# Optimization experiments

Hardware: AMD Instinct MI355X
Metric: run time of the kernel (lower is better)

Reference implementation:

```python
import jax, jax.numpy as jnp
import numpy as np

N0, N1, N2 = 500000, 50000, 4096
E0, E1 = 1280000, 40960
IN, HID, OUT = 128, 256, 47


def _seg_mean(msg, dst, n):
    # scatter-mean of messages into n target buckets
    s = jax.ops.segment_sum(msg, dst, num_segments=n)
    cnt = jax.ops.segment_sum(jnp.ones((dst.shape[0],), msg.dtype), dst, num_segments=n)
    return s / jnp.maximum(cnt, 1.0)[:, None]


def _sage_conv(x_src, x_tgt, src, dst, W_l, b_l, W_r, n_tgt):
    # PyG SAGEConv (mean aggr): lin_l(mean_j x_j) + lin_r(x_i); bias on lin_l only
    agg = _seg_mean(x_src[src], dst, n_tgt)           # [n_tgt, d_in]
    return agg @ W_l + b_l + x_tgt @ W_r              # [n_tgt, d_out]


def setup_inputs() -> dict:
    key = jax.random.key(0)
    ks = jax.random.split(key, 9)
    inp = {
        "x": jax.random.normal(ks[0], (N0, IN), dtype=jnp.float32),
        "W_l0": jax.random.normal(ks[1], (IN, HID), dtype=jnp.float32) / np.sqrt(IN),
        "b_l0": jnp.zeros((HID,), dtype=jnp.float32),
        "W_r0": jax.random.normal(ks[2], (IN, HID), dtype=jnp.float32) / np.sqrt(IN),
        "W_l1": jax.random.normal(ks[3], (HID, OUT), dtype=jnp.float32) / np.sqrt(HID),
        "b_l1": jnp.zeros((OUT,), dtype=jnp.float32),
        "W_r1": jax.random.normal(ks[4], (HID, OUT), dtype=jnp.float32) / np.sqrt(HID),
        "src0": jax.random.randint(ks[5], (E0,), 0, N0, dtype=jnp.int32),
        "dst0": jax.random.randint(ks[6], (E0,), 0, N1, dtype=jnp.int32),
        "src1": jax.random.randint(ks[7], (E1,), 0, N1, dtype=jnp.int32),
        "dst1": jax.random.randint(ks[8], (E1,), 0, N2, dtype=jnp.int32),
        "n1": N1,
        "n2": N2,
    }
    return inp


def reference(x, W_l0, b_l0, W_r0, W_l1, b_l1, W_r1, src0, dst0, src1, dst1, n1, n2):
    # layer 0: bipartite conv (N0 sources -> n1 targets), relu (dropout: eval mode)
    h = _sage_conv(x, x[:n1], src0, dst0, W_l0, b_l0, W_r0, n1)
    h = jax.nn.relu(h)
    # layer 1: (n1 sources -> n2 targets)
    out = _sage_conv(h, h[:n2], src1, dst1, W_l1, b_l1, W_r1, n2)
    return jax.nn.log_softmax(out, axis=-1)
```

## Files before the change

### kernel.cpp

```cpp
#include <hip/hip_runtime.h>
#include <math.h>

typedef unsigned int u32;
typedef short bf16x8 __attribute__((ext_vector_type(8)));
typedef float f32x4 __attribute__((ext_vector_type(4)));

#define N0V 500000
#define N1V 50000
#define N2V 4096
#define E0V 1280000
#define E1V 40960
#define INF 128
#define HIDF 256
#define OUTF 47

#define HIST_BLOCKS 5160
#define PACKW_BLOCKS 128
#define USEDT_BLOCKS 16
#define USEDS_BLOCKS 160

#define NB0 196
#define NB1 16

__device__ __forceinline__ u32 bf16rne(float f) {
  u32 u = __float_as_uint(f);
  return (u + 0x7fffu + ((u >> 16) & 1u)) >> 16;
}
__device__ __forceinline__ u32 pk2(float lo, float hi) {
  return bf16rne(lo) | (bf16rne(hi) << 16);
}

__global__ __launch_bounds__(256) void prep_k(
    const int* __restrict__ dst0, const int* __restrict__ dst1,
    const int* __restrict__ src1,
    int* __restrict__ hist0, int* __restrict__ hist1, int* __restrict__ used,
    const float* __restrict__ Wl, const float* __restrict__ Wr,
    u32* __restrict__ Wf) {
  const int b = blockIdx.x;
  const int tid = threadIdx.x;
  if (b < HIST_BLOCKS) {
    int gid = b * 256 + tid;
    if (gid < E0V) {
      atomicAdd(&hist0[dst0[gid]], 1);
    } else {
      atomicAdd(&hist1[dst1[gid - E0V]], 1);
    }
  } else if (b < HIST_BLOCKS + PACKW_BLOCKS) {
    int gid = (b - HIST_BLOCKS) * 256 + tid;
    int e0 = 2 * gid;
    int j = e0 & 7;
    int lane = (e0 >> 3) & 63;
    int sq = e0 >> 9;
    int s = sq & 7;
    int t = sq >> 3;
    int n = t * 16 + (lane & 15);
    int k0 = s * 32 + (lane >> 4) * 8 + j;
    float v0 = (k0 < 128) ? Wl[k0 * 256 + n] : Wr[(k0 - 128) * 256 + n];
    float v1 = (k0 + 1 < 128) ? Wl[(k0 + 1) * 256 + n] : Wr[(k0 + 1 - 128) * 256 + n];
    Wf[gid] = pk2(v0, v1);
  } else if (b < HIST_BLOCKS + PACKW_BLOCKS + USEDT_BLOCKS) {
    int gid = (b - HIST_BLOCKS - PACKW_BLOCKS) * 256 + tid;
    used[gid] = 1;
  } else {
    int gid = (b - HIST_BLOCKS - PACKW_BLOCKS - USEDT_BLOCKS) * 256 + tid;
    used[src1[gid]] = 1;
  }
}

__global__ __launch_bounds__(256) void scanpart_k(
    const int* __restrict__ hist0, const int* __restrict__ hist1,
    const int* __restrict__ used,
    int* __restrict__ blkpc, int* __restrict__ blku, int* __restrict__ blk1) {
  __shared__ int sA[256], sB[256];
  const int b = blockIdx.x, t = threadIdx.x;
  if (b < NB0) {
    int i = b * 256 + t;
    int pc = 0, u = 0;
    if (i < N1V) {
      u = used[i];
      pc = u ? ((hist0[i] + 15) & ~15) : 0;
    }
    sA[t] = pc; sB[t] = u;
    __syncthreads();
    for (int off = 128; off > 0; off >>= 1) {
      if (t < off) { sA[t] += sA[t + off]; sB[t] += sB[t + off]; }
      __syncthreads();
    }
    if (t == 0) { blkpc[b] = sA[0]; blku[b] = sB[0]; }
  } else {
    int i = (b - NB0) * 256 + t;
    sA[t] = hist1[i];
    __syncthreads();
    for (int off = 128; off > 0; off >>= 1) {
      if (t < off) sA[t] += sA[t + off];
      __syncthreads();
    }
    if (t == 0) blk1[b - NB0] = sA[0];
  }
}

__global__ __launch_bounds__(256) void scanapply_k(
    const int* __restrict__ hist0, const int* __restrict__ hist1,
    const int* __restrict__ used,
    const int* __restrict__ blkpc, const int* __restrict__ blku,
    const int* __restrict__ blk1,
    int* __restrict__ poff, int* __restrict__ cntc,
    int* __restrict__ rowof, int* __restrict__ map,
    int* __restrict__ cur0, int* __restrict__ off1, int* __restrict__ cur1,
    int* __restrict__ Ucnt) {
  __shared__ int sA[256], sB[256];
  const int b = blockIdx.x, t = threadIdx.x;
  if (b < NB0) {
    sA[t] = (t < NB0) ? blkpc[t] : 0;
    sB[t] = (t < NB0) ? blku[t] : 0;
    __syncthreads();
    for (int off = 1; off < 256; off <<= 1) {
      int va = (t >= off) ? sA[t - off] : 0;
      int vb = (t >= off) ? sB[t - off] : 0;
      __syncthreads();
      sA[t] += va; sB[t] += vb;
      __syncthreads();
    }
    int base_pc = (b > 0) ? sA[b - 1] : 0;
    int base_u  = (b > 0) ? sB[b - 1] : 0;
    int total_pc = sA[255];
    int U = sB[255];
    __syncthreads();
    int i = b * 256 + t;
    int u = 0, n = 0, pc = 0;
    if (i < N1V) {
      u = used[i];
      n = u ? hist0[i] : 0;
      pc = u ? ((n + 15) & ~15) : 0;
    }
    sA[t] = pc; sB[t] = u;
    __syncthreads();
    for (int off = 1; off < 256; off <<= 1) {
      int va = (t >= off) ? sA[t - off] : 0;
      int vb = (t >= off) ? sB[t - off] : 0;
      __syncthreads();
      sA[t] += va; sB[t] += vb;
      __syncthreads();
    }
    if (u) {
      int j = base_u + sB[t] - u;
      int p = base_pc + sA[t] - pc;
      map[i] = j;
      rowof[j] = i;
      poff[j] = p;
      cntc[j] = n;
      cur0[i] = p;
    }
    if (b == NB0 - 1 && t == 0) {
      Ucnt[0] = U;
      for (int k = 0; k <= 16; k++) poff[U + k] = total_pc;
      for (int k = 0; k < 16; k++) cntc[U + k] = 0;
    }
  } else {
    int bb = b - NB0;
    sA[t] = (t < NB1) ? blk1[t] : 0;
    __syncthreads();
    for (int off = 1; off < 256; off <<= 1) {
      int va = (t >= off) ? sA[t - off] : 0;
      __syncthreads();
      sA[t] += va;
      __syncthreads();
    }
    int base = (bb > 0) ? sA[bb - 1] : 0;
    int total = sA[255];
    __syncthreads();
    int i = bb * 256 + t;
    int c = hist1[i];
    sA[t] = c;
    __syncthreads();
    for (int off = 1; off < 256; off <<= 1) {
      int va = (t >= off) ? sA[t - off] : 0;
      __syncthreads();
      sA[t] += va;
      __syncthreads();
    }
    int o = base + sA[t] - c;
    off1[i] = o; cur1[i] = o;
    if (bb == NB1 - 1 && t == 255) off1[N2V] = total;
  }
}

__global__ __launch_bounds__(256) void scatteridx_k(
    const int* __restrict__ src0, const int* __restrict__ dst0,
    const int* __restrict__ src1, const int* __restrict__ dst1,
    const int* __restrict__ used, const int* __restrict__ map,
    int* __restrict__ cur0, int* __restrict__ cur1,
    int* __restrict__ esrc0, int* __restrict__ esrc1) {
  int gid = blockIdx.x * 256 + threadIdx.x;
  if (gid < E0V) {
    int d = dst0[gid];
    if (used[d]) {
      int pos = atomicAdd(&cur0[d], 1);
      esrc0[pos] = src0[gid];
    }
  } else if (gid < E0V + E1V) {
    int g = gid - E0V;
    int pos = atomicAdd(&cur1[dst1[g]], 1);
    esrc1[pos] = map[src1[g]];
  }
}

__global__ __launch_bounds__(256) void dense0_mfma(
    const float* __restrict__ x,
    const int* __restrict__ poff, const int* __restrict__ cntc,
    const int* __restrict__ rowof, const int* __restrict__ esrc0,
    const int* __restrict__ Ucnt,
    const u32* __restrict__ Wf, const float* __restrict__ bl,
    float* __restrict__ h) {
  const int U = Ucnt[0];
  const int base = blockIdx.x * 16;
  if (base >= U) return;
  __shared__ __align__(16) unsigned short A_lds[16][264];
  const int tid = threadIdx.x;
  const int wave = __builtin_amdgcn_readfirstlane(tid >> 6);
  const int lane = tid & 63;

  {
    int r = tid >> 4;
    int j = base + r;
    int cg = (tid & 15) * 8;
    if (j < U) {
      int row = rowof[j];
      const float4* xp = (const float4*)(x + row * INF + cg);
      float4 a = xp[0], b = xp[1];
      u32 o[4];
      o[0] = pk2(a.x, a.y); o[1] = pk2(a.z, a.w);
      o[2] = pk2(b.x, b.y); o[3] = pk2(b.z, b.w);
      *(uint4*)&A_lds[r][128 + cg] = *(const uint4*)o;
    } else {
      uint4 z = {0u, 0u, 0u, 0u};
      *(uint4*)&A_lds[r][128 + cg] = z;
    }
  }

  const int half = lane >> 5;
  const int w = lane & 31;
  const float4* xr = (const float4*)x;
  const float4 x0 = xr[w];

  const int r0 = base + wave * 4;
  const int p0 = __builtin_amdgcn_readfirstlane(poff[r0]);
  const int c1 = __builtin_amdgcn_readfirstlane(poff[r0 + 1]) - p0;
  const int c2 = __builtin_amdgcn_readfirstlane(poff[r0 + 2]) - p0;
  const int c3 = __builtin_amdgcn_readfirstlane(poff[r0 + 3]) - p0;
  const int m  = __builtin_amdgcn_readfirstlane(poff[r0 + 4]) - p0;
  const int* e = esrc0 + p0;

  f32x4 acc[4];
#pragma unroll
  for (int q = 0; q < 4; q++) acc[q] = (f32x4){0.f, 0.f, 0.f, 0.f};

#define LOADIDS(ID, st)                                                 \
  _Pragma("unroll") for (int u = 0; u < 8; u++) ID[u] = e[(st) + 2 * u + half];
#define ISSUE(V, ID)                                                    \
  _Pragma("unroll") for (int u = 0; u < 8; u++) V[u] = xr[ID[u] * 32 + w];
#define ADDTO(Q, sx, sy, sz, sw_)                                       \
  { acc[Q][0] += sx; acc[Q][1] += sy; acc[Q][2] += sz; acc[Q][3] += sw_; }
#define ACCUM(V, st)                                                    \
  {                                                                     \
    float sx = 0.f, sy = 0.f, sz = 0.f, sw_ = 0.f;                      \
    _Pragma("unroll") for (int u = 0; u < 8; u++) {                     \
      sx += V[u].x; sy += V[u].y; sz += V[u].z; sw_ += V[u].w;          \
    }                                                                   \
    if ((st) < c1) ADDTO(0, sx, sy, sz, sw_)                            \
    else if ((st) < c2) ADDTO(1, sx, sy, sz, sw_)                       \
    else if ((st) < c3) ADDTO(2, sx, sy, sz, sw_)                       \
    else ADDTO(3, sx, sy, sz, sw_)                                      \
  }

  if (m > 0) {
    int iA[8], iB[8];
    float4 vA[8], vB[8];
    const int nch = m >> 4;
    LOADIDS(iA, 0)
    ISSUE(vA, iA)
    if (nch > 1) LOADIDS(iB, 16)
    int cc = 0;
    for (; cc + 2 <= nch; cc += 2) {
      ISSUE(vB, iB)
      ACCUM(vA, cc * 16)
      if (cc + 2 < nch) {
        LOADIDS(iA, (cc + 2) * 16)
        ISSUE(vA, iA)
      }
      if (cc + 3 < nch) LOADIDS(iB, (cc + 3) * 16)
      ACCUM(vB, (cc + 1) * 16)
    }
    if (cc < nch) ACCUM(vA, cc * 16)
  }
#undef LOADIDS
#undef ISSUE
#undef ADDTO
#undef ACCUM

  {
    const int n0 = __builtin_amdgcn_readfirstlane(cntc[r0]);
    const int n1 = __builtin_amdgcn_readfirstlane(cntc[r0 + 1]);
    const int n2 = __builtin_amdgcn_readfirstlane(cntc[r0 + 2]);
    const int n3 = __builtin_amdgcn_readfirstlane(cntc[r0 + 3]);
    int nq[4] = {n0, n1, n2, n3};
    int pq[4] = {c1 - n0, (c2 - c1) - n1, (c3 - c2) - n2, (m - c3) - n3};
#pragma unroll
    for (int q = 0; q < 4; q++) {
      float sx = acc[q][0] + __shfl_xor(acc[q][0], 32, 64);
      float sy = acc[q][1] + __shfl_xor(acc[q][1], 32, 64);
      float sz = acc[q][2] + __shfl_xor(acc[q][2], 32, 64);
      float sw = acc[q][3] + __shfl_xor(acc[q][3], 32, 64);
      float fp = (float)pq[q];
      sx -= fp * x0.x; sy -= fp * x0.y; sz -= fp * x0.z; sw -= fp * x0.w;
      float rinv = 1.f / fmaxf((float)nq[q], 1.f);
      if (half == 0) {
        uint2 p;
        p.x = pk2(sx * rinv, sy * rinv);
        p.y = pk2(sz * rinv, sw * rinv);
        *(uint2*)&A_lds[wave * 4 + q][4 * w] = p;
      }
    }
  }
  __syncthreads();

  const int mr = lane & 15;
  const int quad = lane >> 4;
  f32x4 oacc[4];
#pragma unroll
  for (int ti = 0; ti < 4; ti++) oacc[ti] = (f32x4){0.f, 0.f, 0.f, 0.f};

  const bf16x8* Wf8 = (const bf16x8*)Wf;
  for (int s = 0; s < 8; s++) {
    bf16x8 af = *(const bf16x8*)&A_lds[mr][s * 32 + quad * 8];
#pragma unroll
    for (int ti = 0; ti < 4; ti++) {
      int t = wave * 4 + ti;
      bf16x8 bfr = Wf8[(t * 8 + s) * 64 + lane];
      oacc[ti] = __builtin_amdgcn_mfma_f32_16x16x32_bf16(af, bfr, oacc[ti], 0, 0, 0);
    }
  }

#pragma unroll
  for (int ti = 0; ti < 4; ti++) {
    int t = wave * 4 + ti;
    int n = t * 16 + mr;
    float b = bl[n];
#pragma unroll
    for (int reg = 0; reg < 4; reg++) {
      int j = base + quad * 4 + reg;
      if (j < U) h[j * HIDF + n] = fmaxf(oacc[ti][reg] + b, 0.0f);
    }
  }
}

__global__ __launch_bounds__(64) void final_fused(
    const float* __restrict__ h, const int* __restrict__ off1,
    const int* __restrict__ esrc1, const float* __restrict__ Wl,
    const float* __restrict__ bl, const float* __restrict__ Wr,
    float* __restrict__ out) {
  __shared__ float a_s[256];
  __shared__ float h_s[256];
  const int i = blockIdx.x;
  const int lane = threadIdx.x;

  int s0 = __builtin_amdgcn_readfirstlane(off1[i]);
  int n  = __builtin_amdgcn_readfirstlane(off1[i + 1]) - s0;
  const int* e = esrc1 + s0;
  const float4* h4 = (const float4*)h;
  float ax = 0.f, ay = 0.f, az = 0.f, aw = 0.f;
  int j = 0;
  for (; j + 4 <= n; j += 4) {
    float4 v[4];
#pragma unroll
    for (int u = 0; u < 4; u++) v[u] = h4[e[j + u] * 64 + lane];
#pragma unroll
    for (int u = 0; u < 4; u++) {
      ax += v[u].x; ay += v[u].y; az += v[u].z; aw += v[u].w;
    }
  }
  for (; j < n; j++) {
    float4 v = h4[e[j] * 64 + lane];
    ax += v.x; ay += v.y; az += v.z; aw += v.w;
  }
  float rinv = 1.f / fmaxf((float)n, 1.f);
  float4 am; am.x = ax * rinv; am.y = ay * rinv; am.z = az * rinv; am.w = aw * rinv;
  ((float4*)a_s)[lane] = am;
  ((float4*)h_s)[lane] = h4[i * 64 + lane];
  __syncthreads();

  float val = -INFINITY;
  if (lane < OUTF) {
    float acc = bl[lane];
#pragma unroll 4
    for (int k = 0; k < 256; k++)
      acc += a_s[k] * Wl[k * OUTF + lane] + h_s[k] * Wr[k * OUTF + lane];
    val = acc;
  }

  float mx = val;
  for (int off = 32; off >= 1; off >>= 1) mx = fmaxf(mx, __shfl_xor(mx, off, 64));
  float ex = (lane < OUTF) ? expf(val - mx) : 0.0f;
  float ssum = ex;
  for (int off = 32; off >= 1; off >>= 1) ssum += __shfl_xor(ssum, off, 64);

  if (lane < OUTF) out[i * OUTF + lane] = val - mx - logf(ssum);
}

extern "C" void kernel_launch(void* const* d_in, const int* in_sizes, int n_in,
                              void* d_out, int out_size, void* d_ws, size_t ws_size,
                              hipStream_t stream) {
  const float* x   = (const float*)d_in[0];
  const float* Wl0 = (const float*)d_in[1];
  const float* bl0 = (const float*)d_in[2];
  const float* Wr0 = (const float*)d_in[3];
  const float* Wl1 = (const float*)d_in[4];
  const float* bl1 = (const float*)d_in[5];
  const float* Wr1 = (const float*)d_in[6];
  const int* src0  = (const int*)d_in[7];
  const int* dst0  = (const int*)d_in[8];
  const int* src1  = (const int*)d_in[9];
  const int* dst1  = (const int*)d_in[10];
  float* out = (float*)d_out;

  char* ws = (char*)d_ws;
  int* hist0 = (int*)(ws);
  int* hist1 = (int*)(ws + 200064);
  int* used  = (int*)(ws + 216448);
  int* esrc0 = (int*)(ws + 416448);
  int* poff  = (int*)(ws + 7216448);
  int* cntc  = (int*)(ws + 7416576);
  int* rowof = (int*)(ws + 7616640);
  int* map   = (int*)(ws + 7816704);
  int* cur0  = (int*)(ws + 8016704);
  int* off1  = (int*)(ws + 8216704);
  int* cur1  = (int*)(ws + 8233152);
  int* esrc1 = (int*)(ws + 8249536);
  int* Ucnt  = (int*)(ws + 8413376);
  int* blkpc = (int*)(ws + 8413440);
  int* blku  = (int*)(ws + 8414464);
  int* blk1  = (int*)(ws + 8415488);
  float* h   = (float*)(ws + 8416640);
  u32* Wf0   = (u32*)(ws + 59616640);

  hipMemsetAsync(ws, 0, 7216448, stream);

  prep_k<<<HIST_BLOCKS + PACKW_BLOCKS + USEDT_BLOCKS + USEDS_BLOCKS, 256, 0, stream>>>(
      dst0, dst1, src1, hist0, hist1, used, Wl0, Wr0, Wf0);
  scanpart_k<<<NB0 + NB1, 256, 0, stream>>>(hist0, hist1, used, blkpc, blku, blk1);
  scanapply_k<<<NB0 + NB1, 256, 0, stream>>>(hist0, hist1, used, blkpc, blku, blk1,
                                             poff, cntc, rowof, map, cur0, off1, cur1,
                                             Ucnt);
  scatteridx_k<<<(E0V + E1V + 255) / 256, 256, 0, stream>>>(
      src0, dst0, src1, dst1, used, map, cur0, cur1, esrc0, esrc1);
  dense0_mfma<<<N1V / 16, 256, 0, stream>>>(x, poff, cntc, rowof, esrc0, Ucnt,
                                            Wf0, bl0, h);
  final_fused<<<N2V, 64, 0, stream>>>(h, off1, esrc1, Wl1, bl1, Wr1, out);
}
```

Before: 541.5 us.

## Shrink workspace memset, defer self-row LDS write, split final kernel across two waves

The workspace memset now covers only the histogram and used arrays. The padding entries of esrc0 are zeroed in scanapply_k instead, which avoids clearing about 7 MB each call. In dense0_mfma the self-row loads of x are issued early but packed to bf16 and written to LDS only after the neighbor accumulation, so their latency overlaps the gather. final_fused now runs two waves per target node: each wave gathers half of the edges and half of the K reduction, and the partial sums are combined through LDS, at the cost of extra synchronisation.

Measured after the change: 531.0 us. No clear change (-1.9%).

```diff
diff --git a/kernel.cpp b/kernel.cpp
--- a/kernel.cpp
+++ b/kernel.cpp
@@ -107,7 +107,7 @@
     int* __restrict__ poff, int* __restrict__ cntc,
     int* __restrict__ rowof, int* __restrict__ map,
     int* __restrict__ cur0, int* __restrict__ off1, int* __restrict__ cur1,
-    int* __restrict__ Ucnt) {
+    int* __restrict__ Ucnt, int* __restrict__ esrc0) {
   __shared__ int sA[256], sB[256];
   const int b = blockIdx.x, t = threadIdx.x;
   if (b < NB0) {
@@ -150,6 +150,7 @@
       poff[j] = p;
       cntc[j] = n;
       cur0[i] = p;
+      for (int k = n; k < pc; k++) esrc0[p + k] = 0;
     }
     if (b == NB0 - 1 && t == 0) {
       Ucnt[0] = U;
@@ -220,22 +221,14 @@
   const int wave = __builtin_amdgcn_readfirstlane(tid >> 6);
   const int lane = tid & 63;
 
-  {
-    int r = tid >> 4;
-    int j = base + r;
-    int cg = (tid & 15) * 8;
-    if (j < U) {
-      int row = rowof[j];
-      const float4* xp = (const float4*)(x + row * INF + cg);
-      float4 a = xp[0], b = xp[1];
-      u32 o[4];
-      o[0] = pk2(a.x, a.y); o[1] = pk2(a.z, a.w);
-      o[2] = pk2(b.x, b.y); o[3] = pk2(b.z, b.w);
-      *(uint4*)&A_lds[r][128 + cg] = *(const uint4*)o;
-    } else {
-      uint4 z = {0u, 0u, 0u, 0u};
-      *(uint4*)&A_lds[r][128 + cg] = z;
-    }
+  const int r_self = tid >> 4;
+  const int cg = (tid & 15) * 8;
+  const bool shave = (base + r_self) < U;
+  float4 sfa, sfb;
+  if (shave) {
+    int row = rowof[base + r_self];
+    const float4* xp = (const float4*)(x + row * INF + cg);
+    sfa = xp[0]; sfb = xp[1];
   }
 
   const int half = lane >> 5;
@@ -298,6 +291,16 @@
 #undef ADDTO
 #undef ACCUM
 
+  if (shave) {
+    u32 o[4];
+    o[0] = pk2(sfa.x, sfa.y); o[1] = pk2(sfa.z, sfa.w);
+    o[2] = pk2(sfb.x, sfb.y); o[3] = pk2(sfb.z, sfb.w);
+    *(uint4*)&A_lds[r_self][128 + cg] = *(const uint4*)o;
+  } else {
+    uint4 z = {0u, 0u, 0u, 0u};
+    *(uint4*)&A_lds[r_self][128 + cg] = z;
+  }
+
   {
     const int n0 = __builtin_amdgcn_readfirstlane(cntc[r0]);
     const int n1 = __builtin_amdgcn_readfirstlane(cntc[r0 + 1]);
@@ -354,23 +357,31 @@
   }
 }
 
-__global__ __launch_bounds__(64) void final_fused(
+__global__ __launch_bounds__(128) void final_fused(
     const float* __restrict__ h, const int* __restrict__ off1,
     const int* __restrict__ esrc1, const float* __restrict__ Wl,
     const float* __restrict__ bl, const float* __restrict__ Wr,
     float* __restrict__ out) {
+  __shared__ float a_ws[2][256];
   __shared__ float a_s[256];
   __shared__ float h_s[256];
+  __shared__ float pacc[2][64];
   const int i = blockIdx.x;
-  const int lane = threadIdx.x;
+  const int tid = threadIdx.x;
+  const int wv = __builtin_amdgcn_readfirstlane(tid >> 6);
+  const int lane = tid & 63;
 
   int s0 = __builtin_amdgcn_readfirstlane(off1[i]);
   int n  = __builtin_amdgcn_readfirstlane(off1[i + 1]) - s0;
   const int* e = esrc1 + s0;
   const float4* h4 = (const float4*)h;
+
+  const int nh = n >> 1;
+  const int lo = wv ? nh : 0;
+  const int hi = wv ? n : nh;
   float ax = 0.f, ay = 0.f, az = 0.f, aw = 0.f;
-  int j = 0;
-  for (; j + 4 <= n; j += 4) {
+  int j = lo;
+  for (; j + 4 <= hi; j += 4) {
     float4 v[4];
 #pragma unroll
     for (int u = 0; u < 4; u++) v[u] = h4[e[j + u] * 64 + lane];
@@ -379,32 +390,41 @@
       ax += v[u].x; ay += v[u].y; az += v[u].z; aw += v[u].w;
     }
   }
-  for (; j < n; j++) {
+  for (; j < hi; j++) {
     float4 v = h4[e[j] * 64 + lane];
     ax += v.x; ay += v.y; az += v.z; aw += v.w;
   }
+  float4 am; am.x = ax; am.y = ay; am.z = az; am.w = aw;
+  ((float4*)a_ws[wv])[lane] = am;
+  if (wv == 0) ((float4*)h_s)[lane] = h4[i * 64 + lane];
+  __syncthreads();
+
   float rinv = 1.f / fmaxf((float)n, 1.f);
-  float4 am; am.x = ax * rinv; am.y = ay * rinv; am.z = az * rinv; am.w = aw * rinv;
-  ((float4*)a_s)[lane] = am;
-  ((float4*)h_s)[lane] = h4[i * 64 + lane];
+  a_s[tid] = (a_ws[0][tid] + a_ws[1][tid]) * rinv;
+  a_s[tid + 128] = (a_ws[0][tid + 128] + a_ws[1][tid + 128]) * rinv;
   __syncthreads();
 
-  float val = -INFINITY;
-  if (lane < OUTF) {
-    float acc = bl[lane];
+  {
+    float acc = (wv == 0 && lane < OUTF) ? bl[lane] : 0.f;
+    if (lane < OUTF) {
+      const int k0 = wv * 128;
 #pragma unroll 4
-    for (int k = 0; k < 256; k++)
-      acc += a_s[k] * Wl[k * OUTF + lane] + h_s[k] * Wr[k * OUTF + lane];
-    val = acc;
-  }
-
-  float mx = val;
-  for (int off = 32; off >= 1; off >>= 1) mx = fmaxf(mx, __shfl_xor(mx, off, 64));
-  float ex = (lane < OUTF) ? expf(val - mx) : 0.0f;
-  float ssum = ex;
-  for (int off = 32; off >= 1; off >>= 1) ssum += __shfl_xor(ssum, off, 64);
-
-  if (lane < OUTF) out[i * OUTF + lane] = val - mx - logf(ssum);
+      for (int k = k0; k < k0 + 128; k++)
+        acc += a_s[k] * Wl[k * OUTF + lane] + h_s[k] * Wr[k * OUTF + lane];
+    }
+    pacc[wv][lane] = acc;
+  }
+  __syncthreads();
+
+  if (wv == 0) {
+    float val = (lane < OUTF) ? (pacc[0][lane] + pacc[1][lane]) : -INFINITY;
+    float mx = val;
+    for (int off = 32; off >= 1; off >>= 1) mx = fmaxf(mx, __shfl_xor(mx, off, 64));
+    float ex = (lane < OUTF) ? expf(val - mx) : 0.0f;
+    float ssum = ex;
+    for (int off = 32; off >= 1; off >>= 1) ssum += __shfl_xor(ssum, off, 64);
+    if (lane < OUTF) out[i * OUTF + lane] = val - mx - logf(ssum);
+  }
 }
 
 extern "C" void kernel_launch(void* const* d_in, const int* in_sizes, int n_in,
@@ -443,17 +463,17 @@
   float* h   = (float*)(ws + 8416640);
   u32* Wf0   = (u32*)(ws + 59616640);
 
-  hipMemsetAsync(ws, 0, 7216448, stream);
+  hipMemsetAsync(ws, 0, 416448, stream);
 
   prep_k<<<HIST_BLOCKS + PACKW_BLOCKS + USEDT_BLOCKS + USEDS_BLOCKS, 256, 0, stream>>>(
       dst0, dst1, src1, hist0, hist1, used, Wl0, Wr0, Wf0);
   scanpart_k<<<NB0 + NB1, 256, 0, stream>>>(hist0, hist1, used, blkpc, blku, blk1);
   scanapply_k<<<NB0 + NB1, 256, 0, stream>>>(hist0, hist1, used, blkpc, blku, blk1,
                                              poff, cntc, rowof, map, cur0, off1, cur1,
-                                             Ucnt);
+                                             Ucnt, esrc0);
   scatteridx_k<<<(E0V + E1V + 255) / 256, 256, 0, stream>>>(
       src0, dst0, src1, dst1, used, map, cur0, cur1, esrc0, esrc1);
   dense0_mfma<<<N1V / 16, 256, 0, stream>>>(x, poff, cntc, rowof, esrc0, Ucnt,
                                             Wf0, bl0, h);
-  final_fused<<<N2V, 64, 0, stream>>>(h, off1, esrc1, Wl1, bl1, Wr1, out);
-}
+  final_fused<<<N2V, 128, 0, stream>>>(h, off1, esrc1, Wl1, bl1, Wr1, out);
+}
```
